# Optimization experiments

Measured on AMD Instinct MI355X. Metric: run time of the kernel, lower is better.

Reference implementation:

```python
import jax, jax.numpy as jnp
import numpy as np

NUM_HEADS = 32
NUM_KV_HEADS = 8
HEAD_DIM = 128
ROPE_THETA = 10000.0


def rotate_half(x):
    half = x.shape[-1] // 2
    return jnp.concatenate((-x[..., half:], x[..., :half]), axis=-1)


def setup_inputs() -> dict:
    key = jax.random.key(0)
    k1, k2, k3 = jax.random.split(key, 3)
    B, S, H = 2, 2048, 4096
    qkv_out = (NUM_KV_HEADS * 2 + NUM_HEADS) * HEAD_DIM  # 6144
    hidden_states = jax.random.normal(k1, (B, S, H), dtype=jnp.float32)
    position_ids = jnp.broadcast_to(jnp.arange(S, dtype=jnp.int64 if jax.config.jax_enable_x64 else jnp.int32)[None, :], (B, S))
    w_qkv = jax.random.normal(k2, (qkv_out, H), dtype=jnp.float32) * (1.0 / np.sqrt(H))
    w_dense = jax.random.normal(k3, (H, H), dtype=jnp.float32) * (1.0 / np.sqrt(H))
    return {"hidden_states": hidden_states, "position_ids": position_ids, "w_qkv": w_qkv, "w_dense": w_dense}


def reference(hidden_states, position_ids, w_qkv, w_dense):
    B, S, H = hidden_states.shape
    nh, nkv, hd = NUM_HEADS, NUM_KV_HEADS, HEAD_DIM
    g = nh // nkv  # query heads per kv head

    # fused QKV projection (FalconLinear, no bias)
    fused = hidden_states @ w_qkv.T  # [B, S, (nkv*(g+2))*hd]

    # new_decoder_architecture split: [B, S, nkv, g+2, hd]
    qkv = fused.reshape(B, S, nkv, g + 2, hd)
    q = qkv[:, :, :, :-2]                 # [B, S, nkv, g, hd]
    k = qkv[:, :, :, -2:-1]               # [B, S, nkv, 1, hd]
    v = qkv[:, :, :, -1:]
    k = jnp.broadcast_to(k, q.shape)      # GQA broadcast to all query heads
    v = jnp.broadcast_to(v, q.shape)
    # flatten kv-head/group dims -> [B, S, nh, hd], then [B, nh, S, hd]
    q = q.reshape(B, S, nh, hd).transpose(0, 2, 1, 3)
    k = k.reshape(B, S, nh, hd).transpose(0, 2, 1, 3)
    v = v.reshape(B, S, nh, hd).transpose(0, 2, 1, 3)

    # default RoPE (attention_scaling = 1.0)
    inv_freq = 1.0 / (ROPE_THETA ** (jnp.arange(0, hd, 2, dtype=jnp.float32) / hd))  # [hd/2]
    freqs = position_ids.astype(jnp.float32)[:, :, None] * inv_freq[None, None, :]   # [B, S, hd/2]
    emb = jnp.concatenate((freqs, freqs), axis=-1)                                    # [B, S, hd]
    cos = jnp.cos(emb)[:, None].astype(hidden_states.dtype)                           # [B, 1, S, hd]
    sin = jnp.sin(emb)[:, None].astype(hidden_states.dtype)
    q = q * cos + rotate_half(q) * sin
    k = k * cos + rotate_half(k) * sin

    # causal SDPA
    scale = 1.0 / np.sqrt(hd)
    scores = jnp.einsum('bhqd,bhkd->bhqk', q, k) * scale  # [B, nh, S, S]
    causal = jnp.tril(jnp.ones((S, S), dtype=bool))
    scores = jnp.where(causal[None, None], scores, jnp.finfo(scores.dtype).min)
    attn = jax.nn.softmax(scores, axis=-1)
    ctx = jnp.einsum('bhqk,bhkd->bhqd', attn, v)          # [B, nh, S, hd]

    # merge heads + output dense
    ctx = ctx.transpose(0, 2, 1, 3).reshape(B, S, nh * hd)
    return ctx @ w_dense.T
```

## Files before the change

### kernel.cpp

```cpp
#include <hip/hip_runtime.h>

typedef __bf16 bf16_t;
typedef __bf16 bf16x8 __attribute__((ext_vector_type(8)));
typedef __bf16 bf16x4 __attribute__((ext_vector_type(4)));
typedef __bf16 bf16x2 __attribute__((ext_vector_type(2)));
typedef float  f32x4  __attribute__((ext_vector_type(4)));
typedef float  f32x16 __attribute__((ext_vector_type(16)));
typedef unsigned int u32x4 __attribute__((ext_vector_type(4)));

#define MFMA16(a, b, c) __builtin_amdgcn_mfma_f32_16x16x32_bf16((a), (b), (c), 0, 0, 0)
#define MFMA32(a, b, c) __builtin_amdgcn_mfma_f32_32x32x16_bf16((a), (b), (c), 0, 0, 0)

__device__ __forceinline__ void async_load16(const void* g, void* l) {
    __builtin_amdgcn_global_load_lds(
        (const __attribute__((address_space(1))) void*)g,
        (__attribute__((address_space(3))) void*)l, 16, 0, 0);
}

__device__ __forceinline__ unsigned pack2(float a, float b) {
    bf16x2 t;
    t[0] = (bf16_t)a;
    t[1] = (bf16_t)b;
    return __builtin_bit_cast(unsigned, t);
}

__global__ void cvt3_f32_to_bf16(const float* __restrict__ s0, bf16_t* __restrict__ d0, int n0,
                                 const float* __restrict__ s1, bf16_t* __restrict__ d1, int n1,
                                 const float* __restrict__ s2, bf16_t* __restrict__ d2, int n2) {
    const float* s; bf16_t* d; int n, bl, nb;
    const int bid = blockIdx.x;
    if (bid < 512)       { s = s0; d = d0; n = n0; bl = bid;        nb = 512; }
    else if (bid < 1280) { s = s1; d = d1; n = n1; bl = bid - 512;  nb = 768; }
    else                 { s = s2; d = d2; n = n2; bl = bid - 1280; nb = 512; }
    const int stride4 = nb * blockDim.x * 4;
    for (int j = (bl * blockDim.x + threadIdx.x) * 4; j < n; j += stride4) {
        float4 v = *(const float4*)(s + j);
        bf16x4 o = { (bf16_t)v.x, (bf16_t)v.y, (bf16_t)v.z, (bf16_t)v.w };
        *(bf16x4*)(d + j) = o;
    }
}

__device__ __forceinline__ void storeC(float* C, size_t idx, float v)  { C[idx] = v; }
__device__ __forceinline__ void storeC(bf16_t* C, size_t idx, float v) { C[idx] = (bf16_t)v; }

__global__ __launch_bounds__(512, 2) void gemm_qkv(const bf16_t* __restrict__ A,
                                                   const bf16_t* __restrict__ B,
                                                   bf16_t* __restrict__ C,
                                                   int M, int N, int K) {
    __shared__ __align__(16) bf16_t ldsA[2][256][64];
    __shared__ __align__(16) bf16_t ldsB[2][192][64];
    const int tid  = threadIdx.x;
    const int lane = tid & 63;
    const int wid  = tid >> 6;
    const int lrow = lane & 15, lhi = lane >> 4;
    const int wrow = (wid >> 1) * 64;
    const int wcol = (wid & 1) * 96;
    const int NT = K >> 6;

    const int nwg = gridDim.x;
    const int w = ((int)blockIdx.x & 7) * (nwg >> 3) + ((int)blockIdx.x >> 3);
    const int nbx = N / 384;
    const size_t m0 = (size_t)(w / nbx) * 256;
    const size_t n0b = (size_t)(w % nbx) * 384;

    const int cm = (((lrow & 1) << 5) | ((lrow & 2) << 3) | ((lrow & 4) << 1));

    const bf16_t* Am = A + m0 * K;

    auto stageA = [&](int bufi, int k0) {
#pragma unroll
        for (int c = 0; c < 4; ++c) {
            int q = tid + 512 * c;
            int row = q >> 3, slot = q & 7;
            int gc = (slot * 8) ^ (((row & 1) << 5) | ((row & 2) << 3) | ((row & 4) << 1));
            async_load16(Am + (size_t)row * K + k0 + gc, &ldsA[bufi][0][0] + q * 8);
        }
    };
    auto stageB = [&](const bf16_t* Bn, int bufi, int k0) {
#pragma unroll
        for (int c = 0; c < 3; ++c) {
            int q = tid + 512 * c;
            int row = q >> 3, slot = q & 7;
            int gc = (slot * 8) ^ (((row & 1) << 5) | ((row & 2) << 3) | ((row & 4) << 1));
            async_load16(Bn + (size_t)row * K + k0 + gc, &ldsB[bufi][0][0] + q * 8);
        }
    };

    for (int half = 0; half < 2; ++half) {
        const bf16_t* Bn = B + (n0b + half * 192) * K;

        f32x4 acc[4][6];
        const f32x4 vz = {0.f, 0.f, 0.f, 0.f};
#pragma unroll
        for (int i = 0; i < 4; ++i)
#pragma unroll
            for (int j = 0; j < 6; ++j) acc[i][j] = vz;

        stageA(0, 0);
        stageB(Bn, 0, 0);
        stageA(1, 64);
        stageB(Bn, 1, 64);
        asm volatile("s_waitcnt vmcnt(7)" ::: "memory");
        __builtin_amdgcn_s_barrier();

        for (int u = 0; u < NT; ++u) {
            const int cur = u & 1;
            __builtin_amdgcn_s_setprio(1);
#pragma unroll
            for (int kk = 0; kk < 2; ++kk) {
                const int cb = kk * 32 + lhi * 8;
                bf16x8 af[4], bfv[6];
#pragma unroll
                for (int i = 0; i < 4; ++i)
                    af[i] = *(const bf16x8*)(&ldsA[cur][wrow + i * 16 + lrow][0] + (cb ^ cm));
#pragma unroll
                for (int j = 0; j < 6; ++j)
                    bfv[j] = *(const bf16x8*)(&ldsB[cur][wcol + j * 16 + lrow][0] + (cb ^ cm));
#pragma unroll
                for (int i = 0; i < 4; ++i)
#pragma unroll
                    for (int j = 0; j < 6; ++j)
                        acc[i][j] = MFMA16(af[i], bfv[j], acc[i][j]);
            }
            __builtin_amdgcn_s_setprio(0);
            __builtin_amdgcn_s_barrier();
            if (u + 2 < NT) {
                stageA(cur, (u + 2) * 64);
                stageB(Bn, cur, (u + 2) * 64);
            }
            if (u == NT - 2)     asm volatile("s_waitcnt vmcnt(0)" ::: "memory");
            else if (u < NT - 2) asm volatile("s_waitcnt vmcnt(7)" ::: "memory");
            __builtin_amdgcn_s_barrier();
        }

#pragma unroll
        for (int i = 0; i < 4; ++i)
#pragma unroll
            for (int j = 0; j < 6; ++j)
#pragma unroll
                for (int r = 0; r < 4; ++r) {
                    size_t row = m0 + wrow + i * 16 + lhi * 4 + r;
                    size_t col = n0b + half * 192 + wcol + j * 16 + lrow;
                    C[row * (size_t)N + col] = (bf16_t)acc[i][j][r];
                }
    }
}

template <typename OT>
__global__ __launch_bounds__(512, 2) void gemm256(const bf16_t* __restrict__ A,
                                                  const bf16_t* __restrict__ B,
                                                  OT* __restrict__ C,
                                                  int M, int N, int K) {
    __shared__ __align__(16) bf16_t lds[2][2][2][128][64];
    const int tid  = threadIdx.x;
    const int lane = tid & 63;
    const int wid  = tid >> 6;
    const int lrow = lane & 15, lhi = lane >> 4;
    const int wrow = (wid >> 2) * 64;
    const int wcol = (wid & 3) * 32;
    const int NT = K >> 6;
    const int nbx = N >> 8;

    const int nwg = gridDim.x;
    const int w = ((int)blockIdx.x & 7) * (nwg >> 3) + ((int)blockIdx.x >> 3);
    const size_t m0 = (size_t)(w / nbx) * 256;
    const size_t n0 = (size_t)(w % nbx) * 256;

    const int cmask = ((lrow & 1) << 5) | ((lrow & 2) << 3) | ((lrow & 4) << 1);
    const int cK0 = (lhi * 8) ^ cmask;
    const int cK1 = (32 + lhi * 8) ^ cmask;
    const int r8 = lane >> 3;
    const int gcol = ((lane & 7) * 8) ^ (((r8 & 1) << 5) | ((r8 & 2) << 3) | ((r8 & 4) << 1));

    auto stage = [&](const bf16_t* srcBase, bf16_t* region) {
#pragma unroll
        for (int c = 0; c < 2; ++c)
            async_load16(srcBase + (size_t)(c * 64 + wid * 8 + r8) * K + gcol,
                         region + c * 4096 + wid * 512);
    };

    int buf = 0;
    bf16x8 af[2][4];
    bf16x8 b0f[2][2], b1f[2][2];

    auto loadA = [&](int mh) {
#pragma unroll
        for (int i = 0; i < 4; ++i) {
            const bf16_t* rp = &lds[buf][0][mh][wrow + i * 16 + lrow][0];
            af[0][i] = *(const bf16x8*)(rp + cK0);
            af[1][i] = *(const bf16x8*)(rp + cK1);
        }
    };
    auto loadB = [&](int nh, bf16x8 (&bf)[2][2]) {
#pragma unroll
        for (int j = 0; j < 2; ++j) {
            const bf16_t* rp = &lds[buf][1][nh][wcol + j * 16 + lrow][0];
            bf[0][j] = *(const bf16x8*)(rp + cK0);
            bf[1][j] = *(const bf16x8*)(rp + cK1);
        }
    };
    auto mmacc = [&](f32x4 (&acc)[4][2], bf16x8 (&bf)[2][2]) {
#pragma unroll
        for (int kk = 0; kk < 2; ++kk)
#pragma unroll
            for (int i = 0; i < 4; ++i)
#pragma unroll
                for (int j = 0; j < 2; ++j)
                    acc[i][j] = MFMA16(af[kk][i], bf[kk][j], acc[i][j]);
    };

    f32x4 a00[4][2], a01[4][2], a10[4][2], a11[4][2];
    const f32x4 vz = {0.f, 0.f, 0.f, 0.f};
#pragma unroll
    for (int i = 0; i < 4; ++i)
#pragma unroll
        for (int j = 0; j < 2; ++j) { a00[i][j] = vz; a01[i][j] = vz; a10[i][j] = vz; a11[i][j] = vz; }

    const bf16_t* Am = A + m0 * K;
    const bf16_t* Bn = B + n0 * K;

    stage(Am,                     &lds[0][0][0][0][0]);
    stage(Bn,                     &lds[0][1][0][0][0]);
    stage(Bn + (size_t)128 * K,   &lds[0][1][1][0][0]);
    stage(Am + (size_t)128 * K,   &lds[0][0][1][0][0]);
    stage(Am + 64,                &lds[1][0][0][0][0]);
    stage(Bn + 64,                &lds[1][1][0][0][0]);
    asm volatile("s_waitcnt vmcnt(4)" ::: "memory");
    __builtin_amdgcn_s_barrier();

    for (int u = 0; u < NT; ++u, buf ^= 1) {
        loadA(0);
        loadB(0, b0f);
        loadB(1, b1f);
        __builtin_amdgcn_s_barrier();
        asm volatile("s_waitcnt lgkmcnt(0)" ::: "memory");
        if (u + 1 < NT) {
            stage(Bn + (size_t)(u + 1) * 64 + (size_t)128 * K, &lds[buf ^ 1][1][1][0][0]);
            stage(Am + (size_t)(u + 1) * 64 + (size_t)128 * K, &lds[buf ^ 1][0][1][0][0]);
        }
        __builtin_amdgcn_s_setprio(1);
        mmacc(a00, b0f);
        mmacc(a01, b1f);
        __builtin_amdgcn_s_setprio(0);
        __builtin_amdgcn_s_barrier();
        loadA(1);
        __builtin_amdgcn_s_barrier();
        asm volatile("s_waitcnt lgkmcnt(0)" ::: "memory");
        if (u + 2 < NT) {
            stage(Am + (size_t)(u + 2) * 64, &lds[buf][0][0][0][0]);
            stage(Bn + (size_t)(u + 2) * 64, &lds[buf][1][0][0][0]);
        }
        __builtin_amdgcn_s_setprio(1);
        mmacc(a10, b0f);
        mmacc(a11, b1f);
        __builtin_amdgcn_s_setprio(0);
        if (u == NT - 2)     asm volatile("s_waitcnt vmcnt(0)" ::: "memory");
        else if (u < NT - 2) asm volatile("s_waitcnt vmcnt(4)" ::: "memory");
        __builtin_amdgcn_s_barrier();
    }

    auto storeQ = [&](f32x4 (&acc)[4][2], int mq, int nq) {
#pragma unroll
        for (int i = 0; i < 4; ++i)
#pragma unroll
            for (int j = 0; j < 2; ++j)
#pragma unroll
                for (int r = 0; r < 4; ++r) {
                    size_t row = m0 + mq * 128 + wrow + i * 16 + lhi * 4 + r;
                    size_t col = n0 + nq * 128 + wcol + j * 16 + lrow;
                    storeC(C, row * (size_t)N + col, acc[i][j][r]);
                }
    };
    storeQ(a00, 0, 0); storeQ(a01, 0, 1); storeQ(a10, 1, 0); storeQ(a11, 1, 1);
}

__global__ void rope_scatter(const bf16_t* __restrict__ fused, const int* __restrict__ pos_ids,
                             bf16_t* __restrict__ Q, bf16_t* __restrict__ Kb) {
    const int token = blockIdx.x;
    const int b = token >> 11, s = token & 2047;
    const int d = threadIdx.x;
    const float pos = (float)pos_ids[token];
    const float inv = __expf(-(float)d * (9.210340371976184f / 64.0f));
    float sn, c;
    sincosf(pos * inv, &sn, &c);
    const bf16_t* frow = fused + (size_t)token * 6144;
    for (int it = 0; it < 5; ++it) {
        int ss = it * 8 + threadIdx.y;
        int col;
        bf16_t* outp;
        if (ss < 32) {
            int h = ss, kv = h >> 2, gi = h & 3;
            col  = kv * 768 + gi * 128 + d;
            outp = Q + (((size_t)b * 32 + h) * 2048 + s) * 128 + d;
        } else {
            int kv = ss - 32;
            col  = kv * 768 + 512 + d;
            outp = Kb + (((size_t)b * 8 + kv) * 2048 + s) * 128 + d;
        }
        float x0 = (float)frow[col];
        float x1 = (float)frow[col + 64];
        outp[0]  = (bf16_t)(x0 * c - x1 * sn);
        outp[64] = (bf16_t)(x1 * c + x0 * sn);
    }
}

__global__ void v_transpose(const bf16_t* __restrict__ fused, bf16_t* __restrict__ Vt) {
    __shared__ bf16_t tile[32][33];
    const int s0 = blockIdx.x * 32;
    const int d0 = blockIdx.y * 32;
    const int bk = blockIdx.z;
    const int b = bk >> 3, kv = bk & 7;
    const int col0 = kv * 768 + 640 + d0;
    const int tx = threadIdx.x, ty = threadIdx.y;
#pragma unroll
    for (int i = 0; i < 4; i++) {
        int sy = ty + i * 8;
        tile[sy][tx] = fused[((size_t)b * 2048 + s0 + sy) * 6144 + col0 + tx];
    }
    __syncthreads();
#pragma unroll
    for (int i = 0; i < 4; i++) {
        int dy = ty + i * 8;
        Vt[((size_t)bk * 128 + d0 + dy) * 2048 + s0 + tx] = tile[tx][dy];
    }
}

__global__ __launch_bounds__(256) void attn_fwd6(const bf16_t* __restrict__ Q,
                                                 const bf16_t* __restrict__ Kb,
                                                 const bf16_t* __restrict__ Vt,
                                                 bf16_t* __restrict__ ctx) {
    __shared__ __align__(16) bf16_t Ks[2][32][128];
    __shared__ __align__(16) bf16_t Vs[2][128][32];
    const int tid  = threadIdx.x;
    const int lane = tid & 63;
    const int wid  = tid >> 6;
    const int l31  = lane & 31;
    const int hi   = lane >> 5;

    const int bidx  = blockIdx.x;
    const int slot  = bidx >> 8;
    const int rr    = (bidx >> 4) & 15;
    const int combo = bidx & 15;
    const int b     = combo & 1;
    const int kvh   = combo >> 1;
    int qt;
    switch (slot) {
        case 0: qt = rr;      break;
        case 1: qt = 63 - rr; break;
        case 2: qt = 16 + rr; break;
        default: qt = 47 - rr; break;
    }
    const int q0 = qt * 32;
    const int h  = kvh * 4 + wid;

    const bf16_t* kbase = Kb + (((size_t)b * 8 + kvh) * 2048) * 128;
    const bf16_t* vbase = Vt + (((size_t)b * 8 + kvh) * 128) * 2048;
    const float kl = 0.12750062133361622f;

    auto stageKV = [&](int bufi, int kv0) {
#pragma unroll
        for (int c = 0; c < 2; ++c) {
            int q = tid + 256 * c;
            int r = q >> 4;
            int cl = ((q & 15) * 16) ^ ((r & 7) << 4);
            async_load16(kbase + (size_t)(kv0 + r) * 128 + (cl >> 1),
                         &Ks[bufi][0][0] + q * 8);
        }
#pragma unroll
        for (int c = 0; c < 2; ++c) {
            int q = tid + 256 * c;
            int d = q >> 2;
            int cl = ((q & 3) * 16) ^ ((d & 3) << 4);
            async_load16(vbase + (size_t)d * 2048 + kv0 + (cl >> 1),
                         &Vs[bufi][0][0] + q * 8);
        }
    };

    const bf16_t* qbase = Q + (((size_t)b * 32 + h) * 2048 + q0) * 128;
    bf16x8 qf[8];
#pragma unroll
    for (int kc = 0; kc < 8; ++kc)
        qf[kc] = *(const bf16x8*)(qbase + (size_t)l31 * 128 + kc * 16 + hi * 8);

    f32x16 o[4];
#pragma unroll
    for (int db = 0; db < 4; ++db)
#pragma unroll
        for (int r = 0; r < 16; ++r) o[db][r] = 0.f;
    float m = -1e30f, lsum = 0.f;

    const int kxor = (l31 & 7) << 3;
    const int vxor = (l31 & 3) << 3;

    stageKV(0, 0);
    __syncthreads();

    int buf = 0;
    for (int st = 0; st <= qt; ++st, buf ^= 1) {
        if (st < qt) stageKV(buf ^ 1, (st + 1) * 32);

        const bf16_t* krow = &Ks[buf][l31][0];
        f32x16 s;
#pragma unroll
        for (int r = 0; r < 16; ++r) s[r] = 0.f;
#pragma unroll
        for (int kc = 0; kc < 8; kc += 2) {
            bf16x8 k0 = *(const bf16x8*)(krow + ((kc * 16 + hi * 8) ^ kxor));
            bf16x8 k1 = *(const bf16x8*)(krow + (((kc + 1) * 16 + hi * 8) ^ kxor));
            s = MFMA32(k0, qf[kc], s);
            s = MFMA32(k1, qf[kc + 1], s);
        }

        if (st == qt) {
            const int qg = q0 + l31;
            const int kv0 = st * 32;
#pragma unroll
            for (int r = 0; r < 16; ++r) {
                int kvg = kv0 + (r & 3) + 8 * (r >> 2) + 4 * hi;
                if (kvg > qg) s[r] = -1e30f;
            }
        }
        float mx01 = fmaxf(s[0], s[1]);
#pragma unroll
        for (int r = 2; r < 16; r += 2) mx01 = fmaxf(mx01, fmaxf(s[r], s[r + 1]));
        float pmax = fmaxf(mx01, __shfl_xor(mx01, 32, 64));
        if (pmax > m + 90.5f) {
            float corr = exp2f((m - pmax) * kl);
            lsum *= corr;
#pragma unroll
            for (int db = 0; db < 4; ++db)
#pragma unroll
                for (int r = 0; r < 16; ++r) o[db][r] *= corr;
            m = pmax;
        }
        const float mk = m * kl;
        float ps4[4] = {0.f, 0.f, 0.f, 0.f};
#pragma unroll
        for (int r = 0; r < 16; ++r) {
            float e = exp2f(fmaf(s[r], kl, -mk));
            s[r] = e;
            ps4[r & 3] += e;
        }
        lsum += (ps4[0] + ps4[1]) + (ps4[2] + ps4[3]);

#pragma unroll
        for (int ks = 0; ks < 2; ++ks) {
            unsigned u0 = pack2(s[ks * 8 + 0], s[ks * 8 + 1]);
            unsigned u1 = pack2(s[ks * 8 + 2], s[ks * 8 + 3]);
            unsigned u2 = pack2(s[ks * 8 + 4], s[ks * 8 + 5]);
            unsigned u3 = pack2(s[ks * 8 + 6], s[ks * 8 + 7]);
            unsigned t0 = __shfl_xor(u0, 32, 64);
            unsigned t1 = __shfl_xor(u1, 32, 64);
            unsigned t2 = __shfl_xor(u2, 32, 64);
            unsigned t3 = __shfl_xor(u3, 32, 64);
            u32x4 uw;
            uw[0] = hi ? t2 : u0;
            uw[1] = hi ? t3 : u1;
            uw[2] = hi ? u2 : t0;
            uw[3] = hi ? u3 : t1;
            bf16x8 pb = __builtin_bit_cast(bf16x8, uw);
            const int vcol = (ks * 16 + hi * 8) ^ vxor;
#pragma unroll
            for (int db = 0; db < 4; ++db) {
                bf16x8 vf = *(const bf16x8*)(&Vs[buf][db * 32 + l31][0] + vcol);
                o[db] = MFMA32(vf, pb, o[db]);
            }
        }
        __syncthreads();
    }

    float lall = lsum + __shfl_xor(lsum, 32, 64);
    const float inv = 1.0f / lall;
    bf16_t* cb = ctx + ((size_t)(b * 2048 + q0 + l31)) * 4096 + h * 128;
#pragma unroll
    for (int db = 0; db < 4; ++db)
#pragma unroll
        for (int g = 0; g < 4; ++g) {
            bf16x4 w;
#pragma unroll
            for (int i = 0; i < 4; ++i) w[i] = (bf16_t)(o[db][g * 4 + i] * inv);
            *(bf16x4*)(cb + db * 32 + g * 8 + hi * 4) = w;
        }
}

extern "C" void kernel_launch(void* const* d_in, const int* in_sizes, int n_in,
                              void* d_out, int out_size, void* d_ws, size_t ws_size,
                              hipStream_t stream) {
    const float* hs   = (const float*)d_in[0];
    const int*   pos  = (const int*)d_in[1];
    const float* wqkv = (const float*)d_in[2];
    const float* wd   = (const float*)d_in[3];
    float* out = (float*)d_out;
    char* ws = (char*)d_ws;

    bf16_t* Xb    = (bf16_t*)(ws + 0ull);
    bf16_t* Wqkvb = (bf16_t*)(ws + 33554432ull);
    bf16_t* Wdb   = (bf16_t*)(ws + 83886080ull);
    bf16_t* fused = (bf16_t*)(ws + 117440512ull);
    bf16_t* Kb    = (bf16_t*)(ws + 167772160ull);
    bf16_t* Vt    = (bf16_t*)(ws + 176160768ull);
    bf16_t* Qb    = Xb;
    bf16_t* ctx   = fused;

    cvt3_f32_to_bf16<<<1792, 256, 0, stream>>>(hs, Xb, 16777216,
                                               wqkv, Wqkvb, 25165824,
                                               wd, Wdb, 16777216);

    gemm_qkv<<<256, 512, 0, stream>>>(Xb, Wqkvb, fused, 4096, 6144, 4096);

    rope_scatter<<<4096, dim3(64, 8), 0, stream>>>(fused, pos, Qb, Kb);
    v_transpose<<<dim3(64, 4, 16), dim3(32, 8), 0, stream>>>(fused, Vt);

    attn_fwd6<<<1024, 256, 0, stream>>>(Qb, Kb, Vt, ctx);

    gemm256<float><<<256, 512, 0, stream>>>(ctx, Wdb, out, 4096, 4096, 4096);
}
```

Before: 572.3 us.

## Pair complementary causal query tiles per block sharing 64-wide KV staging

```diff
diff --git a/kernel.cpp b/kernel.cpp
--- a/kernel.cpp
+++ b/kernel.cpp
@@ -325,33 +325,31 @@
     }
 }
 
-__global__ __launch_bounds__(256) void attn_fwd6(const bf16_t* __restrict__ Q,
+__global__ __launch_bounds__(512) void attn_fwd7(const bf16_t* __restrict__ Q,
                                                  const bf16_t* __restrict__ Kb,
                                                  const bf16_t* __restrict__ Vt,
                                                  bf16_t* __restrict__ ctx) {
-    __shared__ __align__(16) bf16_t Ks[2][32][128];
-    __shared__ __align__(16) bf16_t Vs[2][128][32];
+    __shared__ __align__(16) bf16_t Ks[2][64][128];
+    __shared__ __align__(16) bf16_t Vs[2][128][64];
     const int tid  = threadIdx.x;
     const int lane = tid & 63;
     const int wid  = tid >> 6;
     const int l31  = lane & 31;
     const int hi   = lane >> 5;
 
-    const int bidx  = blockIdx.x;
-    const int slot  = bidx >> 8;
-    const int rr    = (bidx >> 4) & 15;
-    const int combo = bidx & 15;
+    const int bid   = blockIdx.x;
+    const int combo = bid & 15;
     const int b     = combo & 1;
     const int kvh   = combo >> 1;
-    int qt;
-    switch (slot) {
-        case 0: qt = rr;      break;
-        case 1: qt = 63 - rr; break;
-        case 2: qt = 16 + rr; break;
-        default: qt = 47 - rr; break;
-    }
-    const int q0 = qt * 32;
-    const int h  = kvh * 4 + wid;
+    const int rest  = bid >> 4;
+    const int pp    = rest >> 1;
+    const int p     = (rest & 1) ? pp : 31 - pp;
+    const int qa = p, qb = 63 - p;
+    const int grp = wid >> 2;
+    const int qt  = grp ? qa : qb;
+    const int q0  = qt * 32;
+    const int h   = kvh * 4 + (wid & 3);
+    const int ntiles = (qb >> 1) + 1;
 
     const bf16_t* kbase = Kb + (((size_t)b * 8 + kvh) * 2048) * 128;
     const bf16_t* vbase = Vt + (((size_t)b * 8 + kvh) * 128) * 2048;
@@ -360,7 +358,7 @@
     auto stageKV = [&](int bufi, int kv0) {
 #pragma unroll
         for (int c = 0; c < 2; ++c) {
-            int q = tid + 256 * c;
+            int q = tid + 512 * c;
             int r = q >> 4;
             int cl = ((q & 15) * 16) ^ ((r & 7) << 4);
             async_load16(kbase + (size_t)(kv0 + r) * 128 + (cl >> 1),
@@ -368,9 +366,9 @@
         }
 #pragma unroll
         for (int c = 0; c < 2; ++c) {
-            int q = tid + 256 * c;
-            int d = q >> 2;
-            int cl = ((q & 3) * 16) ^ ((d & 3) << 4);
+            int q = tid + 512 * c;
+            int d = q >> 3;
+            int cl = ((q & 7) * 16) ^ ((d & 3) << 4);
             async_load16(vbase + (size_t)d * 2048 + kv0 + (cl >> 1),
                          &Vs[bufi][0][0] + q * 8);
         }
@@ -396,74 +394,79 @@
     __syncthreads();
 
     int buf = 0;
-    for (int st = 0; st <= qt; ++st, buf ^= 1) {
-        if (st < qt) stageKV(buf ^ 1, (st + 1) * 32);
-
-        const bf16_t* krow = &Ks[buf][l31][0];
-        f32x16 s;
-#pragma unroll
-        for (int r = 0; r < 16; ++r) s[r] = 0.f;
-#pragma unroll
-        for (int kc = 0; kc < 8; kc += 2) {
-            bf16x8 k0 = *(const bf16x8*)(krow + ((kc * 16 + hi * 8) ^ kxor));
-            bf16x8 k1 = *(const bf16x8*)(krow + (((kc + 1) * 16 + hi * 8) ^ kxor));
-            s = MFMA32(k0, qf[kc], s);
-            s = MFMA32(k1, qf[kc + 1], s);
-        }
-
-        if (st == qt) {
-            const int qg = q0 + l31;
-            const int kv0 = st * 32;
+    for (int t = 0; t < ntiles; ++t, buf ^= 1) {
+        if (t + 1 < ntiles) stageKV(buf ^ 1, (t + 1) * 64);
+
+#pragma unroll
+        for (int sub = 0; sub < 2; ++sub) {
+            const int kvg0 = t * 64 + sub * 32;
+            if (kvg0 > q0 + 31) continue;
+
+            const bf16_t* krow = &Ks[buf][sub * 32 + l31][0];
+            f32x16 s;
+#pragma unroll
+            for (int r = 0; r < 16; ++r) s[r] = 0.f;
+#pragma unroll
+            for (int kc = 0; kc < 8; kc += 2) {
+                bf16x8 k0 = *(const bf16x8*)(krow + ((kc * 16 + hi * 8) ^ kxor));
+                bf16x8 k1 = *(const bf16x8*)(krow + (((kc + 1) * 16 + hi * 8) ^ kxor));
+                s = MFMA32(k0, qf[kc], s);
+                s = MFMA32(k1, qf[kc + 1], s);
+            }
+
+            if (kvg0 + 31 > q0) {
+                const int qg = q0 + l31;
+#pragma unroll
+                for (int r = 0; r < 16; ++r) {
+                    int kvg = kvg0 + (r & 3) + 8 * (r >> 2) + 4 * hi;
+                    if (kvg > qg) s[r] = -1e30f;
+                }
+            }
+            float mx01 = fmaxf(s[0], s[1]);
+#pragma unroll
+            for (int r = 2; r < 16; r += 2) mx01 = fmaxf(mx01, fmaxf(s[r], s[r + 1]));
+            float pmax = fmaxf(mx01, __shfl_xor(mx01, 32, 64));
+            if (pmax > m + 90.5f) {
+                float corr = exp2f((m - pmax) * kl);
+                lsum *= corr;
+#pragma unroll
+                for (int db = 0; db < 4; ++db)
+#pragma unroll
+                    for (int r = 0; r < 16; ++r) o[db][r] *= corr;
+                m = pmax;
+            }
+            const float mk = m * kl;
+            float ps4[4] = {0.f, 0.f, 0.f, 0.f};
 #pragma unroll
             for (int r = 0; r < 16; ++r) {
-                int kvg = kv0 + (r & 3) + 8 * (r >> 2) + 4 * hi;
-                if (kvg > qg) s[r] = -1e30f;
-            }
-        }
-        float mx01 = fmaxf(s[0], s[1]);
-#pragma unroll
-        for (int r = 2; r < 16; r += 2) mx01 = fmaxf(mx01, fmaxf(s[r], s[r + 1]));
-        float pmax = fmaxf(mx01, __shfl_xor(mx01, 32, 64));
-        if (pmax > m + 90.5f) {
-            float corr = exp2f((m - pmax) * kl);
-            lsum *= corr;
-#pragma unroll
-            for (int db = 0; db < 4; ++db)
-#pragma unroll
-                for (int r = 0; r < 16; ++r) o[db][r] *= corr;
-            m = pmax;
-        }
-        const float mk = m * kl;
-        float ps4[4] = {0.f, 0.f, 0.f, 0.f};
-#pragma unroll
-        for (int r = 0; r < 16; ++r) {
-            float e = exp2f(fmaf(s[r], kl, -mk));
-            s[r] = e;
-            ps4[r & 3] += e;
-        }
-        lsum += (ps4[0] + ps4[1]) + (ps4[2] + ps4[3]);
-
-#pragma unroll
-        for (int ks = 0; ks < 2; ++ks) {
-            unsigned u0 = pack2(s[ks * 8 + 0], s[ks * 8 + 1]);
-            unsigned u1 = pack2(s[ks * 8 + 2], s[ks * 8 + 3]);
-            unsigned u2 = pack2(s[ks * 8 + 4], s[ks * 8 + 5]);
-            unsigned u3 = pack2(s[ks * 8 + 6], s[ks * 8 + 7]);
-            unsigned t0 = __shfl_xor(u0, 32, 64);
-            unsigned t1 = __shfl_xor(u1, 32, 64);
-            unsigned t2 = __shfl_xor(u2, 32, 64);
-            unsigned t3 = __shfl_xor(u3, 32, 64);
-            u32x4 uw;
-            uw[0] = hi ? t2 : u0;
-            uw[1] = hi ? t3 : u1;
-            uw[2] = hi ? u2 : t0;
-            uw[3] = hi ? u3 : t1;
-            bf16x8 pb = __builtin_bit_cast(bf16x8, uw);
-            const int vcol = (ks * 16 + hi * 8) ^ vxor;
-#pragma unroll
-            for (int db = 0; db < 4; ++db) {
-                bf16x8 vf = *(const bf16x8*)(&Vs[buf][db * 32 + l31][0] + vcol);
-                o[db] = MFMA32(vf, pb, o[db]);
+                float e = exp2f(fmaf(s[r], kl, -mk));
+                s[r] = e;
+                ps4[r & 3] += e;
+            }
+            lsum += (ps4[0] + ps4[1]) + (ps4[2] + ps4[3]);
+
+#pragma unroll
+            for (int ks = 0; ks < 2; ++ks) {
+                unsigned u0 = pack2(s[ks * 8 + 0], s[ks * 8 + 1]);
+                unsigned u1 = pack2(s[ks * 8 + 2], s[ks * 8 + 3]);
+                unsigned u2 = pack2(s[ks * 8 + 4], s[ks * 8 + 5]);
+                unsigned u3 = pack2(s[ks * 8 + 6], s[ks * 8 + 7]);
+                unsigned t0 = __shfl_xor(u0, 32, 64);
+                unsigned t1 = __shfl_xor(u1, 32, 64);
+                unsigned t2 = __shfl_xor(u2, 32, 64);
+                unsigned t3 = __shfl_xor(u3, 32, 64);
+                u32x4 uw;
+                uw[0] = hi ? t2 : u0;
+                uw[1] = hi ? t3 : u1;
+                uw[2] = hi ? u2 : t0;
+                uw[3] = hi ? u3 : t1;
+                bf16x8 pb = __builtin_bit_cast(bf16x8, uw);
+                const int vcol = (sub * 32 + ks * 16 + hi * 8) ^ vxor;
+#pragma unroll
+                for (int db = 0; db < 4; ++db) {
+                    bf16x8 vf = *(const bf16x8*)(&Vs[buf][db * 32 + l31][0] + vcol);
+                    o[db] = MFMA32(vf, pb, o[db]);
+                }
             }
         }
         __syncthreads();
@@ -511,7 +514,7 @@
     rope_scatter<<<4096, dim3(64, 8), 0, stream>>>(fused, pos, Qb, Kb);
     v_transpose<<<dim3(64, 4, 16), dim3(32, 8), 0, stream>>>(fused, Vt);
 
-    attn_fwd6<<<1024, 256, 0, stream>>>(Qb, Kb, Vt, ctx);
+    attn_fwd7<<<512, 512, 0, stream>>>(Qb, Kb, Vt, ctx);
 
     gemm256<float><<<256, 512, 0, stream>>>(ctx, Wdb, out, 4096, 4096, 4096);
 }
```

Result: slower. 587.0 us (+2.6%).

## Restructure dense GEMM to per-wave 64x128 tiles and fuse RoPE with V transpose

Applied to the files above, without the earlier changes.

```diff
diff --git a/kernel.cpp b/kernel.cpp
--- a/kernel.cpp
+++ b/kernel.cpp
@@ -40,9 +40,6 @@
     }
 }
 
-__device__ __forceinline__ void storeC(float* C, size_t idx, float v)  { C[idx] = v; }
-__device__ __forceinline__ void storeC(bf16_t* C, size_t idx, float v) { C[idx] = (bf16_t)v; }
-
 __global__ __launch_bounds__(512, 2) void gemm_qkv(const bf16_t* __restrict__ A,
                                                    const bf16_t* __restrict__ B,
                                                    bf16_t* __restrict__ C,
@@ -146,182 +143,149 @@
     }
 }
 
-template <typename OT>
-__global__ __launch_bounds__(512, 2) void gemm256(const bf16_t* __restrict__ A,
+__global__ __launch_bounds__(512) void gemm_dense(const bf16_t* __restrict__ A,
                                                   const bf16_t* __restrict__ B,
-                                                  OT* __restrict__ C,
+                                                  float* __restrict__ C,
                                                   int M, int N, int K) {
-    __shared__ __align__(16) bf16_t lds[2][2][2][128][64];
+    __shared__ __align__(16) bf16_t ldsA[2][256][64];
+    __shared__ __align__(16) bf16_t ldsB[2][256][64];
     const int tid  = threadIdx.x;
     const int lane = tid & 63;
     const int wid  = tid >> 6;
     const int lrow = lane & 15, lhi = lane >> 4;
-    const int wrow = (wid >> 2) * 64;
-    const int wcol = (wid & 3) * 32;
+    const int wrow = (wid >> 1) * 64;
+    const int wcol = (wid & 1) * 128;
     const int NT = K >> 6;
-    const int nbx = N >> 8;
 
     const int nwg = gridDim.x;
     const int w = ((int)blockIdx.x & 7) * (nwg >> 3) + ((int)blockIdx.x >> 3);
+    const int nbx = N >> 8;
     const size_t m0 = (size_t)(w / nbx) * 256;
     const size_t n0 = (size_t)(w % nbx) * 256;
 
-    const int cmask = ((lrow & 1) << 5) | ((lrow & 2) << 3) | ((lrow & 4) << 1);
-    const int cK0 = (lhi * 8) ^ cmask;
-    const int cK1 = (32 + lhi * 8) ^ cmask;
-    const int r8 = lane >> 3;
-    const int gcol = ((lane & 7) * 8) ^ (((r8 & 1) << 5) | ((r8 & 2) << 3) | ((r8 & 4) << 1));
-
-    auto stage = [&](const bf16_t* srcBase, bf16_t* region) {
-#pragma unroll
-        for (int c = 0; c < 2; ++c)
-            async_load16(srcBase + (size_t)(c * 64 + wid * 8 + r8) * K + gcol,
-                         region + c * 4096 + wid * 512);
-    };
-
-    int buf = 0;
-    bf16x8 af[2][4];
-    bf16x8 b0f[2][2], b1f[2][2];
-
-    auto loadA = [&](int mh) {
-#pragma unroll
-        for (int i = 0; i < 4; ++i) {
-            const bf16_t* rp = &lds[buf][0][mh][wrow + i * 16 + lrow][0];
-            af[0][i] = *(const bf16x8*)(rp + cK0);
-            af[1][i] = *(const bf16x8*)(rp + cK1);
-        }
-    };
-    auto loadB = [&](int nh, bf16x8 (&bf)[2][2]) {
-#pragma unroll
-        for (int j = 0; j < 2; ++j) {
-            const bf16_t* rp = &lds[buf][1][nh][wcol + j * 16 + lrow][0];
-            bf[0][j] = *(const bf16x8*)(rp + cK0);
-            bf[1][j] = *(const bf16x8*)(rp + cK1);
-        }
-    };
-    auto mmacc = [&](f32x4 (&acc)[4][2], bf16x8 (&bf)[2][2]) {
-#pragma unroll
-        for (int kk = 0; kk < 2; ++kk)
-#pragma unroll
-            for (int i = 0; i < 4; ++i)
-#pragma unroll
-                for (int j = 0; j < 2; ++j)
-                    acc[i][j] = MFMA16(af[kk][i], bf[kk][j], acc[i][j]);
-    };
-
-    f32x4 a00[4][2], a01[4][2], a10[4][2], a11[4][2];
-    const f32x4 vz = {0.f, 0.f, 0.f, 0.f};
-#pragma unroll
-    for (int i = 0; i < 4; ++i)
-#pragma unroll
-        for (int j = 0; j < 2; ++j) { a00[i][j] = vz; a01[i][j] = vz; a10[i][j] = vz; a11[i][j] = vz; }
+    const int cm = (((lrow & 1) << 5) | ((lrow & 2) << 3) | ((lrow & 4) << 1));
 
     const bf16_t* Am = A + m0 * K;
     const bf16_t* Bn = B + n0 * K;
 
-    stage(Am,                     &lds[0][0][0][0][0]);
-    stage(Bn,                     &lds[0][1][0][0][0]);
-    stage(Bn + (size_t)128 * K,   &lds[0][1][1][0][0]);
-    stage(Am + (size_t)128 * K,   &lds[0][0][1][0][0]);
-    stage(Am + 64,                &lds[1][0][0][0][0]);
-    stage(Bn + 64,                &lds[1][1][0][0][0]);
-    asm volatile("s_waitcnt vmcnt(4)" ::: "memory");
+    auto stageP = [&](const bf16_t* src, bf16_t* dst, int k0) {
+#pragma unroll
+        for (int c = 0; c < 4; ++c) {
+            int q = tid + 512 * c;
+            int row = q >> 3, slot = q & 7;
+            int gc = (slot * 8) ^ (((row & 1) << 5) | ((row & 2) << 3) | ((row & 4) << 1));
+            async_load16(src + (size_t)row * K + k0 + gc, dst + q * 8);
+        }
+    };
+
+    f32x4 acc[4][8];
+    const f32x4 vz = {0.f, 0.f, 0.f, 0.f};
+#pragma unroll
+    for (int i = 0; i < 4; ++i)
+#pragma unroll
+        for (int j = 0; j < 8; ++j) acc[i][j] = vz;
+
+    stageP(Am, &ldsA[0][0][0], 0);
+    stageP(Bn, &ldsB[0][0][0], 0);
+    stageP(Am, &ldsA[1][0][0], 64);
+    stageP(Bn, &ldsB[1][0][0], 64);
+    asm volatile("s_waitcnt vmcnt(8)" ::: "memory");
     __builtin_amdgcn_s_barrier();
 
-    for (int u = 0; u < NT; ++u, buf ^= 1) {
-        loadA(0);
-        loadB(0, b0f);
-        loadB(1, b1f);
-        __builtin_amdgcn_s_barrier();
-        asm volatile("s_waitcnt lgkmcnt(0)" ::: "memory");
-        if (u + 1 < NT) {
-            stage(Bn + (size_t)(u + 1) * 64 + (size_t)128 * K, &lds[buf ^ 1][1][1][0][0]);
-            stage(Am + (size_t)(u + 1) * 64 + (size_t)128 * K, &lds[buf ^ 1][0][1][0][0]);
-        }
+    for (int u = 0; u < NT; ++u) {
+        const int cur = u & 1;
         __builtin_amdgcn_s_setprio(1);
-        mmacc(a00, b0f);
-        mmacc(a01, b1f);
+#pragma unroll
+        for (int kk = 0; kk < 2; ++kk) {
+            const int cb = kk * 32 + lhi * 8;
+            bf16x8 af[4], bfv[8];
+#pragma unroll
+            for (int i = 0; i < 4; ++i)
+                af[i] = *(const bf16x8*)(&ldsA[cur][wrow + i * 16 + lrow][0] + (cb ^ cm));
+#pragma unroll
+            for (int j = 0; j < 8; ++j)
+                bfv[j] = *(const bf16x8*)(&ldsB[cur][wcol + j * 16 + lrow][0] + (cb ^ cm));
+#pragma unroll
+            for (int i = 0; i < 4; ++i)
+#pragma unroll
+                for (int j = 0; j < 8; ++j)
+                    acc[i][j] = MFMA16(af[i], bfv[j], acc[i][j]);
+        }
         __builtin_amdgcn_s_setprio(0);
         __builtin_amdgcn_s_barrier();
-        loadA(1);
+        if (u + 2 < NT) {
+            stageP(Am, &ldsA[cur][0][0], (u + 2) * 64);
+            stageP(Bn, &ldsB[cur][0][0], (u + 2) * 64);
+        }
+        if (u == NT - 2)     asm volatile("s_waitcnt vmcnt(0)" ::: "memory");
+        else if (u < NT - 2) asm volatile("s_waitcnt vmcnt(8)" ::: "memory");
         __builtin_amdgcn_s_barrier();
-        asm volatile("s_waitcnt lgkmcnt(0)" ::: "memory");
-        if (u + 2 < NT) {
-            stage(Am + (size_t)(u + 2) * 64, &lds[buf][0][0][0][0]);
-            stage(Bn + (size_t)(u + 2) * 64, &lds[buf][1][0][0][0]);
-        }
-        __builtin_amdgcn_s_setprio(1);
-        mmacc(a10, b0f);
-        mmacc(a11, b1f);
-        __builtin_amdgcn_s_setprio(0);
-        if (u == NT - 2)     asm volatile("s_waitcnt vmcnt(0)" ::: "memory");
-        else if (u < NT - 2) asm volatile("s_waitcnt vmcnt(4)" ::: "memory");
-        __builtin_amdgcn_s_barrier();
-    }
-
-    auto storeQ = [&](f32x4 (&acc)[4][2], int mq, int nq) {
-#pragma unroll
-        for (int i = 0; i < 4; ++i)
-#pragma unroll
-            for (int j = 0; j < 2; ++j)
-#pragma unroll
-                for (int r = 0; r < 4; ++r) {
-                    size_t row = m0 + mq * 128 + wrow + i * 16 + lhi * 4 + r;
-                    size_t col = n0 + nq * 128 + wcol + j * 16 + lrow;
-                    storeC(C, row * (size_t)N + col, acc[i][j][r]);
-                }
-    };
-    storeQ(a00, 0, 0); storeQ(a01, 0, 1); storeQ(a10, 1, 0); storeQ(a11, 1, 1);
-}
-
-__global__ void rope_scatter(const bf16_t* __restrict__ fused, const int* __restrict__ pos_ids,
-                             bf16_t* __restrict__ Q, bf16_t* __restrict__ Kb) {
-    const int token = blockIdx.x;
-    const int b = token >> 11, s = token & 2047;
-    const int d = threadIdx.x;
-    const float pos = (float)pos_ids[token];
-    const float inv = __expf(-(float)d * (9.210340371976184f / 64.0f));
-    float sn, c;
-    sincosf(pos * inv, &sn, &c);
-    const bf16_t* frow = fused + (size_t)token * 6144;
-    for (int it = 0; it < 5; ++it) {
-        int ss = it * 8 + threadIdx.y;
-        int col;
-        bf16_t* outp;
-        if (ss < 32) {
-            int h = ss, kv = h >> 2, gi = h & 3;
-            col  = kv * 768 + gi * 128 + d;
-            outp = Q + (((size_t)b * 32 + h) * 2048 + s) * 128 + d;
-        } else {
-            int kv = ss - 32;
-            col  = kv * 768 + 512 + d;
-            outp = Kb + (((size_t)b * 8 + kv) * 2048 + s) * 128 + d;
-        }
-        float x0 = (float)frow[col];
-        float x1 = (float)frow[col + 64];
-        outp[0]  = (bf16_t)(x0 * c - x1 * sn);
-        outp[64] = (bf16_t)(x1 * c + x0 * sn);
-    }
-}
-
-__global__ void v_transpose(const bf16_t* __restrict__ fused, bf16_t* __restrict__ Vt) {
+    }
+
+#pragma unroll
+    for (int i = 0; i < 4; ++i)
+#pragma unroll
+        for (int j = 0; j < 8; ++j)
+#pragma unroll
+            for (int r = 0; r < 4; ++r) {
+                size_t row = m0 + wrow + i * 16 + lhi * 4 + r;
+                size_t col = n0 + wcol + j * 16 + lrow;
+                C[row * (size_t)N + col] = acc[i][j][r];
+            }
+}
+
+__global__ void rope_vt(const bf16_t* __restrict__ fused, const int* __restrict__ pos_ids,
+                        bf16_t* __restrict__ Q, bf16_t* __restrict__ Kb,
+                        bf16_t* __restrict__ Vt) {
     __shared__ bf16_t tile[32][33];
-    const int s0 = blockIdx.x * 32;
-    const int d0 = blockIdx.y * 32;
-    const int bk = blockIdx.z;
-    const int b = bk >> 3, kv = bk & 7;
-    const int col0 = kv * 768 + 640 + d0;
-    const int tx = threadIdx.x, ty = threadIdx.y;
-#pragma unroll
-    for (int i = 0; i < 4; i++) {
-        int sy = ty + i * 8;
-        tile[sy][tx] = fused[((size_t)b * 2048 + s0 + sy) * 6144 + col0 + tx];
-    }
-    __syncthreads();
-#pragma unroll
-    for (int i = 0; i < 4; i++) {
-        int dy = ty + i * 8;
-        Vt[((size_t)bk * 128 + d0 + dy) * 2048 + s0 + tx] = tile[tx][dy];
+    const int bid = blockIdx.x;
+    if (bid < 4096) {
+        const int token = bid;
+        const int b = token >> 11, s = token & 2047;
+        const int d = threadIdx.x & 63;
+        const int y = threadIdx.x >> 6;
+        const float pos = (float)pos_ids[token];
+        const float inv = __expf(-(float)d * (9.210340371976184f / 64.0f));
+        float sn, c;
+        sincosf(pos * inv, &sn, &c);
+        const bf16_t* frow = fused + (size_t)token * 6144;
+        for (int it = 0; it < 10; ++it) {
+            int ss = it * 4 + y;
+            int col;
+            bf16_t* outp;
+            if (ss < 32) {
+                int h = ss, kv = h >> 2, gi = h & 3;
+                col  = kv * 768 + gi * 128 + d;
+                outp = Q + (((size_t)b * 32 + h) * 2048 + s) * 128 + d;
+            } else {
+                int kv = ss - 32;
+                col  = kv * 768 + 512 + d;
+                outp = Kb + (((size_t)b * 8 + kv) * 2048 + s) * 128 + d;
+            }
+            float x0 = (float)frow[col];
+            float x1 = (float)frow[col + 64];
+            outp[0]  = (bf16_t)(x0 * c - x1 * sn);
+            outp[64] = (bf16_t)(x1 * c + x0 * sn);
+        }
+    } else {
+        const int idx = bid - 4096;
+        const int s0 = (idx & 63) * 32;
+        const int d0 = ((idx >> 6) & 3) * 32;
+        const int bk = idx >> 8;
+        const int b = bk >> 3, kv = bk & 7;
+        const int col0 = kv * 768 + 640 + d0;
+        const int tx = threadIdx.x & 31, ty = threadIdx.x >> 5;
+#pragma unroll
+        for (int i = 0; i < 4; i++) {
+            int sy = ty + i * 8;
+            tile[sy][tx] = fused[((size_t)b * 2048 + s0 + sy) * 6144 + col0 + tx];
+        }
+        __syncthreads();
+#pragma unroll
+        for (int i = 0; i < 4; i++) {
+            int dy = ty + i * 8;
+            Vt[((size_t)bk * 128 + d0 + dy) * 2048 + s0 + tx] = tile[tx][dy];
+        }
     }
 }
 
@@ -508,10 +472,9 @@
 
     gemm_qkv<<<256, 512, 0, stream>>>(Xb, Wqkvb, fused, 4096, 6144, 4096);
 
-    rope_scatter<<<4096, dim3(64, 8), 0, stream>>>(fused, pos, Qb, Kb);
-    v_transpose<<<dim3(64, 4, 16), dim3(32, 8), 0, stream>>>(fused, Vt);
+    rope_vt<<<8192, 256, 0, stream>>>(fused, pos, Qb, Kb, Vt);
 
     attn_fwd6<<<1024, 256, 0, stream>>>(Qb, Kb, Vt, ctx);
 
-    gemm256<float><<<256, 512, 0, stream>>>(ctx, Wdb, out, 4096, 4096, 4096);
-}
+    gemm_dense<<<256, 512, 0, stream>>>(ctx, Wdb, out, 4096, 4096, 4096);
+}
```

Measured after the change: 584.7 us. 1.02x slower.

## Merge RoPE scatter and V transpose into one launch; remap QKV GEMM tiles per XCD

Applied to the files above, without the earlier changes.

```diff
diff --git a/kernel.cpp b/kernel.cpp
--- a/kernel.cpp
+++ b/kernel.cpp
@@ -57,11 +57,12 @@
     const int wcol = (wid & 1) * 96;
     const int NT = K >> 6;
 
-    const int nwg = gridDim.x;
-    const int w = ((int)blockIdx.x & 7) * (nwg >> 3) + ((int)blockIdx.x >> 3);
-    const int nbx = N / 384;
-    const size_t m0 = (size_t)(w / nbx) * 256;
-    const size_t n0b = (size_t)(w % nbx) * 384;
+    const int xcd = (int)blockIdx.x & 7;
+    const int idx = (int)blockIdx.x >> 3;
+    const int rowt = (xcd >> 1) * 4 + (idx >> 3);
+    const int colt = (xcd & 1) * 8 + (idx & 7);
+    const size_t m0  = (size_t)rowt * 256;
+    const size_t n0b = (size_t)colt * 384;
 
     const int cm = (((lrow & 1) << 5) | ((lrow & 2) << 3) | ((lrow & 4) << 1));
 
@@ -274,54 +275,58 @@
     storeQ(a00, 0, 0); storeQ(a01, 0, 1); storeQ(a10, 1, 0); storeQ(a11, 1, 1);
 }
 
-__global__ void rope_scatter(const bf16_t* __restrict__ fused, const int* __restrict__ pos_ids,
-                             bf16_t* __restrict__ Q, bf16_t* __restrict__ Kb) {
-    const int token = blockIdx.x;
-    const int b = token >> 11, s = token & 2047;
-    const int d = threadIdx.x;
-    const float pos = (float)pos_ids[token];
-    const float inv = __expf(-(float)d * (9.210340371976184f / 64.0f));
-    float sn, c;
-    sincosf(pos * inv, &sn, &c);
-    const bf16_t* frow = fused + (size_t)token * 6144;
-    for (int it = 0; it < 5; ++it) {
-        int ss = it * 8 + threadIdx.y;
-        int col;
-        bf16_t* outp;
-        if (ss < 32) {
-            int h = ss, kv = h >> 2, gi = h & 3;
-            col  = kv * 768 + gi * 128 + d;
-            outp = Q + (((size_t)b * 32 + h) * 2048 + s) * 128 + d;
-        } else {
-            int kv = ss - 32;
-            col  = kv * 768 + 512 + d;
-            outp = Kb + (((size_t)b * 8 + kv) * 2048 + s) * 128 + d;
-        }
-        float x0 = (float)frow[col];
-        float x1 = (float)frow[col + 64];
-        outp[0]  = (bf16_t)(x0 * c - x1 * sn);
-        outp[64] = (bf16_t)(x1 * c + x0 * sn);
-    }
-}
-
-__global__ void v_transpose(const bf16_t* __restrict__ fused, bf16_t* __restrict__ Vt) {
+__global__ void rope_vt(const bf16_t* __restrict__ fused, const int* __restrict__ pos_ids,
+                        bf16_t* __restrict__ Q, bf16_t* __restrict__ Kb,
+                        bf16_t* __restrict__ Vt) {
     __shared__ bf16_t tile[32][33];
-    const int s0 = blockIdx.x * 32;
-    const int d0 = blockIdx.y * 32;
-    const int bk = blockIdx.z;
-    const int b = bk >> 3, kv = bk & 7;
-    const int col0 = kv * 768 + 640 + d0;
-    const int tx = threadIdx.x, ty = threadIdx.y;
-#pragma unroll
-    for (int i = 0; i < 4; i++) {
-        int sy = ty + i * 8;
-        tile[sy][tx] = fused[((size_t)b * 2048 + s0 + sy) * 6144 + col0 + tx];
-    }
-    __syncthreads();
-#pragma unroll
-    for (int i = 0; i < 4; i++) {
-        int dy = ty + i * 8;
-        Vt[((size_t)bk * 128 + d0 + dy) * 2048 + s0 + tx] = tile[tx][dy];
+    const int bid = blockIdx.x;
+    if (bid < 4096) {
+        const int token = bid;
+        const int b = token >> 11, s = token & 2047;
+        const int d = threadIdx.x & 63;
+        const int y = threadIdx.x >> 6;
+        const float pos = (float)pos_ids[token];
+        const float inv = __expf(-(float)d * (9.210340371976184f / 64.0f));
+        float sn, c;
+        sincosf(pos * inv, &sn, &c);
+        const bf16_t* frow = fused + (size_t)token * 6144;
+        for (int it = 0; it < 10; ++it) {
+            int ss = it * 4 + y;
+            int col;
+            bf16_t* outp;
+            if (ss < 32) {
+                int h = ss, kv = h >> 2, gi = h & 3;
+                col  = kv * 768 + gi * 128 + d;
+                outp = Q + (((size_t)b * 32 + h) * 2048 + s) * 128 + d;
+            } else {
+                int kv = ss - 32;
+                col  = kv * 768 + 512 + d;
+                outp = Kb + (((size_t)b * 8 + kv) * 2048 + s) * 128 + d;
+            }
+            float x0 = (float)frow[col];
+            float x1 = (float)frow[col + 64];
+            outp[0]  = (bf16_t)(x0 * c - x1 * sn);
+            outp[64] = (bf16_t)(x1 * c + x0 * sn);
+        }
+    } else {
+        const int idx = bid - 4096;
+        const int s0 = (idx & 63) * 32;
+        const int d0 = ((idx >> 6) & 3) * 32;
+        const int bk = idx >> 8;
+        const int b = bk >> 3, kv = bk & 7;
+        const int col0 = kv * 768 + 640 + d0;
+        const int tx = threadIdx.x & 31, ty = threadIdx.x >> 5;
+#pragma unroll
+        for (int i = 0; i < 4; i++) {
+            int sy = ty + i * 8;
+            tile[sy][tx] = fused[((size_t)b * 2048 + s0 + sy) * 6144 + col0 + tx];
+        }
+        __syncthreads();
+#pragma unroll
+        for (int i = 0; i < 4; i++) {
+            int dy = ty + i * 8;
+            Vt[((size_t)bk * 128 + d0 + dy) * 2048 + s0 + tx] = tile[tx][dy];
+        }
     }
 }
 
@@ -508,8 +513,7 @@
 
     gemm_qkv<<<256, 512, 0, stream>>>(Xb, Wqkvb, fused, 4096, 6144, 4096);
 
-    rope_scatter<<<4096, dim3(64, 8), 0, stream>>>(fused, pos, Qb, Kb);
-    v_transpose<<<dim3(64, 4, 16), dim3(32, 8), 0, stream>>>(fused, Vt);
+    rope_vt<<<8192, 256, 0, stream>>>(fused, pos, Qb, Kb, Vt);
 
     attn_fwd6<<<1024, 256, 0, stream>>>(Qb, Kb, Vt, ctx);
 
```

Result: no change. 576.2 us, median of 3 (+0.7%).
